# Optimization experiments

Hardware: AMD Instinct MI355X
Metric: run time of the kernel (lower is better)

The kernel has to match this reference:

```python
import jax, jax.numpy as jnp
import numpy as np

NUM_EMBEDDINGS = 512
EMBEDDING_DIM = 64
COMMITMENT_COST = 0.25


def setup_inputs() -> dict:
    key = jax.random.key(0)
    k1, k2 = jax.random.split(key)
    inputs = jax.random.normal(k1, (64, 32, 32, EMBEDDING_DIM), dtype=jnp.float32)
    # nn.Embedding weight init: uniform(-1/K, 1/K)
    codebook = jax.random.uniform(
        k2, (NUM_EMBEDDINGS, EMBEDDING_DIM), dtype=jnp.float32,
        minval=-1.0 / NUM_EMBEDDINGS, maxval=1.0 / NUM_EMBEDDINGS)
    return {"inputs": inputs, "codebook": codebook}


def reference(inputs, codebook):
    D = codebook.shape[1]
    K = codebook.shape[0]
    flat = inputs.reshape(-1, D)  # [N, D]
    # Squared euclidean distances (argmin-equivalent to torch.cdist output)
    d2 = (jnp.sum(flat * flat, axis=1, keepdims=True)
          - 2.0 * (flat @ codebook.T)
          + jnp.sum(codebook * codebook, axis=1))  # [N, K]
    idx = jnp.argmin(d2, axis=1)  # [N]
    # Gather codebook rows (== one-hot @ codebook in the original)
    quantized = codebook[idx].reshape(inputs.shape)
    e_latent_loss = jnp.mean((jax.lax.stop_gradient(quantized) - inputs) ** 2)
    q_latent_loss = jnp.mean((quantized - jax.lax.stop_gradient(inputs)) ** 2)
    loss = q_latent_loss + COMMITMENT_COST * e_latent_loss
    # Straight-through estimator
    quantized_st = inputs + jax.lax.stop_gradient(quantized - inputs)
    # Perplexity from code usage histogram (== mean of one-hot encodings)
    n = flat.shape[0]
    avg_probs = jnp.zeros((K,), dtype=jnp.float32).at[idx].add(1.0) / n
    perplexity = jnp.exp(-jnp.sum(avg_probs * jnp.log(avg_probs + 1e-10)))
    encoding_indices = idx[:, None]  # [N, 1] to match torch unsqueeze(1)
    return (loss, quantized_st, perplexity, encoding_indices)
```

## Files before the change

kernel.cpp:

```cpp
#include <hip/hip_runtime.h>
#include <math.h>

#define K_EMB 512
#define DIM 64
#define NVEC 65536
#define OUT_LOSS 0
#define OUT_Q 1
#define OUT_PERP (1 + NVEC * DIM)
#define OUT_IDX (1 + NVEC * DIM + 1)
#define EPS2 1e-4f
#define FIX_CAP 16
#define GRID_MAIN 2048
#define SSE_SLOTS 32

typedef __attribute__((ext_vector_type(8))) short short8;
typedef __attribute__((ext_vector_type(4))) float float4v;


__device__ __forceinline__ unsigned short bf16_rn(float f) {
    unsigned u = __float_as_uint(f);
    return (unsigned short)((u + 0x7FFFu + ((u >> 16) & 1u)) >> 16);
}

__device__ __forceinline__ float np_pairwise8_sq(const float* v) {
    float r[8];
#pragma unroll
    for (int j = 0; j < 8; ++j) r[j] = __fmul_rn(v[j], v[j]);
#pragma unroll
    for (int i = 8; i < 64; i += 8) {
#pragma unroll
        for (int j = 0; j < 8; ++j) r[j] = __fadd_rn(r[j], __fmul_rn(v[i + j], v[i + j]));
    }
    return __fadd_rn(__fadd_rn(__fadd_rn(r[0], r[1]), __fadd_rn(r[2], r[3])),
                     __fadd_rn(__fadd_rn(r[4], r[5]), __fadd_rn(r[6], r[7])));
}

__device__ __forceinline__ float np_pairwise8_sq_g(const float* g) {
    float x[64];
    const float4* v4 = (const float4*)g;
#pragma unroll
    for (int i = 0; i < 16; ++i) {
        float4 t = v4[i];
        x[4 * i + 0] = t.x; x[4 * i + 1] = t.y; x[4 * i + 2] = t.z; x[4 * i + 3] = t.w;
    }
    float r[8];
#pragma unroll
    for (int j = 0; j < 8; ++j) r[j] = __fmul_rn(x[j], x[j]);
#pragma unroll
    for (int i = 8; i < 64; i += 8) {
#pragma unroll
        for (int j = 0; j < 8; ++j) r[j] = __fadd_rn(r[j], __fmul_rn(x[i + j], x[i + j]));
    }
    return __fadd_rn(__fadd_rn(__fadd_rn(r[0], r[1]), __fadd_rn(r[2], r[3])),
                     __fadd_rn(__fadd_rn(r[4], r[5]), __fadd_rn(r[6], r[7])));
}

__global__ void vq_frag(const float* __restrict__ codebook, float* __restrict__ csq,
                        unsigned short* __restrict__ ahi, unsigned short* __restrict__ alo,
                        float4* __restrict__ csqf, unsigned* __restrict__ hist,
                        double* __restrict__ sse64, unsigned* __restrict__ cnt) {
    const int tid = threadIdx.x;
    if (blockIdx.x < 16) {
        const int id = blockIdx.x * 256 + tid;
        const int t = id >> 7, step = (id >> 6) & 1, lane = id & 63;
        const int m = t * 16 + (lane & 15);
        const int kb = step * 32 + (lane >> 4) * 8;
        const float4* src = (const float4*)(codebook + (m << 6) + kb);
        float4 f0 = src[0], f1 = src[1];
        const float fs[8] = {f0.x, f0.y, f0.z, f0.w, f1.x, f1.y, f1.z, f1.w};
        short8 h, l;
#pragma unroll
        for (int j = 0; j < 8; ++j) {
            unsigned short hv = bf16_rn(fs[j]);
            float lof = fs[j] - __uint_as_float(((unsigned)hv) << 16);
            h[j] = (short)hv;
            l[j] = (short)bf16_rn(lof);
        }
        const int fo = ((t * 2 + step) * 64 + lane) * 8;
        *(short8*)(ahi + fo) = h;
        *(short8*)(alo + fo) = l;
    } else {
        __shared__ float s_csq[512];
#pragma unroll
        for (int r = 0; r < 2; ++r) {
            const int k = tid + 256 * r;
            float v = np_pairwise8_sq_g(codebook + ((size_t)k << 6));
            s_csq[k] = v;
            csq[k] = v;
            hist[k] = 0u;
        }
        if (tid < SSE_SLOTS) sse64[tid] = 0.0;
        if (tid == SSE_SLOTS) *cnt = 0u;
        __syncthreads();
#pragma unroll
        for (int i = 0; i < 8; ++i) {
            const int id = i * 256 + tid;
            const int t = id >> 6, lane = id & 63;
            const int k0 = t * 16 + (lane >> 4) * 4;
            csqf[id] = make_float4(s_csq[k0], s_csq[k0 + 1], s_csq[k0 + 2], s_csq[k0 + 3]);
        }
    }
}

__launch_bounds__(256, 4)
__global__ void vq_main(const float* __restrict__ inputs, const float* __restrict__ codebook,
                        const float* __restrict__ csq, const unsigned short* __restrict__ ahi,
                        const unsigned short* __restrict__ alo, const float4* __restrict__ csqf,
                        unsigned* __restrict__ hist, double* __restrict__ sse64,
                        unsigned* __restrict__ cnt, float* __restrict__ out) {
    __shared__ __align__(16) float s_x[32 * 68];
    __shared__ float s_A[32];
    __shared__ unsigned long long s_t1[4][32];
    __shared__ unsigned long long s_t2[4][32];
    __shared__ unsigned long long s_e[32];
    __shared__ int s_fix[FIX_CAP];
    __shared__ int s_nfix;
    __shared__ float s_w[4];
    __shared__ int s_last;
    __shared__ float s_wsm[8];
    __shared__ double s_sse[SSE_SLOTS];

    const int tid = threadIdx.x;
    const int wave = tid >> 6, lane = tid & 63;
    const int vbase = blockIdx.x * 32;

    if (tid == 0) s_nfix = 0;

    {
        const float4* src = (const float4*)(inputs + ((size_t)vbase << 6));
#pragma unroll
        for (int i = 0; i < 2; ++i) {
            const int f = i * 256 + tid;
            float4 v = src[f];
            *(float4*)&s_x[(f >> 4) * 68 + (f & 15) * 4] = v;
        }
    }
    __syncthreads();

    if (tid < 32) s_A[tid] = np_pairwise8_sq(&s_x[tid * 68]);
    __syncthreads();

    short8 bhi[2][2], blo[2][2];
#pragma unroll
    for (int vt = 0; vt < 2; ++vt) {
        const int vrow = vt * 16 + (lane & 15);
#pragma unroll
        for (int step = 0; step < 2; ++step) {
            const int kb = step * 32 + (lane >> 4) * 8;
            float4 f0 = *(const float4*)&s_x[vrow * 68 + kb];
            float4 f1 = *(const float4*)&s_x[vrow * 68 + kb + 4];
            const float fs[8] = {f0.x, f0.y, f0.z, f0.w, f1.x, f1.y, f1.z, f1.w};
            short8 h, l;
#pragma unroll
            for (int j = 0; j < 8; ++j) {
                unsigned short hv = bf16_rn(fs[j]);
                float lof = fs[j] - __uint_as_float(((unsigned)hv) << 16);
                h[j] = (short)hv;
                l[j] = (short)bf16_rn(lof);
            }
            bhi[vt][step] = h;
            blo[vt][step] = l;
        }
    }

    unsigned long long e1[2] = {~0ULL, ~0ULL}, e2[2] = {~0ULL, ~0ULL};

#pragma unroll 2
    for (int tt = 0; tt < 8; ++tt) {
        const int t = wave * 8 + tt;
        const int fo0 = ((t * 2 + 0) * 64 + lane) * 8;
        const int fo1 = ((t * 2 + 1) * 64 + lane) * 8;
        short8 ah0 = *(const short8*)(ahi + fo0);
        short8 ah1 = *(const short8*)(ahi + fo1);
        short8 al0 = *(const short8*)(alo + fo0);
        short8 al1 = *(const short8*)(alo + fo1);
        float4 cs = csqf[t * 64 + lane];
        const float csr[4] = {cs.x, cs.y, cs.z, cs.w};
#pragma unroll
        for (int vt = 0; vt < 2; ++vt) {
            float4v acc = {0.f, 0.f, 0.f, 0.f};
            acc = __builtin_amdgcn_mfma_f32_16x16x32_bf16(ah0, bhi[vt][0], acc, 0, 0, 0);
            acc = __builtin_amdgcn_mfma_f32_16x16x32_bf16(ah1, bhi[vt][1], acc, 0, 0, 0);
            acc = __builtin_amdgcn_mfma_f32_16x16x32_bf16(ah0, blo[vt][0], acc, 0, 0, 0);
            acc = __builtin_amdgcn_mfma_f32_16x16x32_bf16(ah1, blo[vt][1], acc, 0, 0, 0);
            acc = __builtin_amdgcn_mfma_f32_16x16x32_bf16(al0, bhi[vt][0], acc, 0, 0, 0);
            acc = __builtin_amdgcn_mfma_f32_16x16x32_bf16(al1, bhi[vt][1], acc, 0, 0, 0);
            const float Avt = s_A[vt * 16 + (lane & 15)];
#pragma unroll
            for (int r = 0; r < 4; ++r) {
                float d2 = __fadd_rn(__fsub_rn(Avt, __fmul_rn(2.0f, acc[r])), csr[r]);
                const unsigned k = (unsigned)(t * 16 + (lane >> 4) * 4 + r);
                unsigned long long e = ((unsigned long long)__float_as_uint(d2) << 32) | k;
                if (e < e1[vt]) { e2[vt] = e1[vt]; e1[vt] = e; }
                else if (e < e2[vt]) e2[vt] = e;
            }
        }
    }

#pragma unroll
    for (int vt = 0; vt < 2; ++vt) {
#pragma unroll
        for (int off = 16; off <= 32; off <<= 1) {
            unsigned long long o1 = __shfl_xor(e1[vt], off);
            unsigned long long o2 = __shfl_xor(e2[vt], off);
            if (o1 < e1[vt]) { e2[vt] = (e1[vt] < o2) ? e1[vt] : o2; e1[vt] = o1; }
            else if (o1 < e2[vt]) e2[vt] = o1;
        }
        if (lane < 16) {
            s_t1[wave][vt * 16 + lane] = e1[vt];
            s_t2[wave][vt * 16 + lane] = e2[vt];
        }
    }
    __syncthreads();

    if (tid < 32) {
        unsigned long long E1 = ~0ULL, E2 = ~0ULL;
#pragma unroll
        for (int w = 0; w < 4; ++w) {
            unsigned long long a = s_t1[w][tid], b = s_t2[w][tid];
            if (a < E1) { E2 = (E1 < b) ? E1 : b; E1 = a; }
            else if (a < E2) E2 = a;
        }
        s_e[tid] = E1;
        float b1 = __uint_as_float((unsigned)(E1 >> 32));
        float b2 = __uint_as_float((unsigned)(E2 >> 32));
        if (__fsub_rn(b2, b1) <= EPS2) {
            int pos = atomicAdd(&s_nfix, 1);
            if (pos < FIX_CAP) s_fix[pos] = tid;
        }
    }
    __syncthreads();

    {
        int nf = s_nfix; if (nf > FIX_CAP) nf = FIX_CAP;
        for (int f = wave; f < nf; f += 4) {
            const int vloc = s_fix[f];
            const float* xr = &s_x[vloc * 68];
            const float A = s_A[vloc];
            unsigned long long best = ~0ULL;
#pragma unroll 1
            for (int r8 = 0; r8 < 8; ++r8) {
                const int k = lane * 8 + r8;
                const float* c = codebook + (k << 6);
                float p[8] = {0.f, 0.f, 0.f, 0.f, 0.f, 0.f, 0.f, 0.f};
#pragma unroll
                for (int ii = 0; ii < 64; ii += 8)
#pragma unroll
                    for (int j = 0; j < 8; ++j)
                        p[j] = __builtin_fmaf(xr[ii + j], c[ii + j], p[j]);
                float dot = __fadd_rn(__fadd_rn(__fadd_rn(p[0], p[1]), __fadd_rn(p[2], p[3])),
                                      __fadd_rn(__fadd_rn(p[4], p[5]), __fadd_rn(p[6], p[7])));
                float d2 = __fadd_rn(__fsub_rn(A, __fmul_rn(2.0f, dot)), csq[k]);
                unsigned long long e = ((unsigned long long)__float_as_uint(d2) << 32) | (unsigned)k;
                if (e < best) best = e;
            }
#pragma unroll
            for (int off = 32; off > 0; off >>= 1) {
                unsigned long long o = __shfl_down(best, off);
                if (o < best) best = o;
            }
            if (lane == 0) s_e[vloc] = best;
        }
    }
    __syncthreads();

    if (tid < 32) {
        const unsigned kf = (unsigned)s_e[tid];
        out[OUT_IDX + vbase + tid] = (float)kf;
        atomicAdd(&hist[kf], 1u);
    }
    {
        float4* dst = (float4*)(out + OUT_Q + ((size_t)vbase << 6));
        float es = 0.f;
#pragma unroll
        for (int i = 0; i < 2; ++i) {
            const int f = i * 256 + tid;
            const int row = f >> 4, col = (f & 15) * 4;
            const unsigned k = (unsigned)s_e[row];
            float4 qv = *(const float4*)(codebook + ((size_t)k << 6) + col);
            dst[f] = qv;
            float4 xv = *(const float4*)&s_x[row * 68 + col];
            float d0 = qv.x - xv.x; es = __builtin_fmaf(d0, d0, es);
            float d1 = qv.y - xv.y; es = __builtin_fmaf(d1, d1, es);
            float d2 = qv.z - xv.z; es = __builtin_fmaf(d2, d2, es);
            float d3 = qv.w - xv.w; es = __builtin_fmaf(d3, d3, es);
        }
#pragma unroll
        for (int off = 32; off > 0; off >>= 1) es += __shfl_down(es, off);
        if (lane == 0) s_w[wave] = es;
    }
    __syncthreads();
    if (tid == 0) {
        atomicAdd(&sse64[blockIdx.x & (SSE_SLOTS - 1)],
                  (double)(((s_w[0] + s_w[1]) + (s_w[2] + s_w[3]))));
        asm volatile("s_waitcnt vmcnt(0)" ::: "memory");
        unsigned ticket = atomicAdd(cnt, 1u);
        s_last = (ticket == GRID_MAIN - 1) ? 1 : 0;
    }
    __syncthreads();

    if (s_last) {
        float pr0 = (float)atomicAdd(&hist[tid], 0u) / 65536.0f;
        float v0 = __fmul_rn(pr0, logf(__fadd_rn(pr0, 1e-10f)));
        float pr1 = (float)atomicAdd(&hist[tid + 256], 0u) / 65536.0f;
        float v1 = __fmul_rn(pr1, logf(__fadd_rn(pr1, 1e-10f)));
#pragma unroll
        for (int off = 32; off > 0; off >>= 1) {
            v0 += __shfl_down(v0, off);
            v1 += __shfl_down(v1, off);
        }
        if (lane == 0) { s_wsm[wave] = v0; s_wsm[4 + wave] = v1; }
        if (tid < SSE_SLOTS) s_sse[tid] = atomicAdd(&sse64[tid], 0.0);
        __syncthreads();
        if (tid == 0) {
            float S = 0.f;
#pragma unroll
            for (int i = 0; i < 8; ++i) S += s_wsm[i];
            out[OUT_PERP] = expf(-S);
            double sv = 0.0;
            for (int i = 0; i < SSE_SLOTS; ++i) sv += s_sse[i];
            float m = (float)(sv / 4194304.0);
            out[OUT_LOSS] = __fadd_rn(m, __fmul_rn(0.25f, m));
        }
    }
}

extern "C" void kernel_launch(void* const* d_in, const int* in_sizes, int n_in,
                              void* d_out, int out_size, void* d_ws, size_t ws_size,
                              hipStream_t stream) {
    const float* inputs   = (const float*)d_in[0];
    const float* codebook = (const float*)d_in[1];
    float* out = (float*)d_out;
    float*          csq   = (float*)d_ws;
    double*         sse64 = (double*)((char*)d_ws + 2048);
    unsigned*       cnt   = (unsigned*)((char*)d_ws + 2304);
    unsigned*       hist  = (unsigned*)((char*)d_ws + 2560);
    unsigned short* ahi   = (unsigned short*)((char*)d_ws + 4608);
    unsigned short* alo   = (unsigned short*)((char*)d_ws + 70144);
    float4*         csqf  = (float4*)((char*)d_ws + 135680);

    vq_frag<<<17, 256, 0, stream>>>(codebook, csq, ahi, alo, csqf, hist, sse64, cnt);
    vq_main<<<GRID_MAIN, 256, 0, stream>>>(inputs, codebook, csq, ahi, alo, csqf, hist, sse64, cnt, out);
}
```

Before: 137.1 us.

## Use single-wave blocks covering all codes with software-pipelined codebook fragment loads

Each block now runs one wave that sweeps all 32 codebook tiles instead of splitting them across four waves. This removes the __syncthreads barriers and the cross-wave top-2 merge through shared memory. Fragment loads are double-buffered with a per-block rotation of the starting tile, the row norms come from in-register FMA plus shuffles, and the distance becomes a single fma. The trade-off is more serial MFMA work per wave and fewer waves per block. The changed norm and distance arithmetic may also shift near-tie results, though the fixup path still recomputes ties exactly.

```diff
diff --git a/kernel.cpp b/kernel.cpp
--- a/kernel.cpp
+++ b/kernel.cpp
@@ -102,45 +102,36 @@
     }
 }
 
-__launch_bounds__(256, 4)
+__launch_bounds__(64, 2)
 __global__ void vq_main(const float* __restrict__ inputs, const float* __restrict__ codebook,
                         const float* __restrict__ csq, const unsigned short* __restrict__ ahi,
                         const unsigned short* __restrict__ alo, const float4* __restrict__ csqf,
                         unsigned* __restrict__ hist, double* __restrict__ sse64,
                         unsigned* __restrict__ cnt, float* __restrict__ out) {
     __shared__ __align__(16) float s_x[32 * 68];
-    __shared__ float s_A[32];
-    __shared__ unsigned long long s_t1[4][32];
-    __shared__ unsigned long long s_t2[4][32];
     __shared__ unsigned long long s_e[32];
     __shared__ int s_fix[FIX_CAP];
     __shared__ int s_nfix;
-    __shared__ float s_w[4];
-    __shared__ int s_last;
     __shared__ float s_wsm[8];
     __shared__ double s_sse[SSE_SLOTS];
 
-    const int tid = threadIdx.x;
-    const int wave = tid >> 6, lane = tid & 63;
+    const int lane = threadIdx.x;
     const int vbase = blockIdx.x * 32;
 
-    if (tid == 0) s_nfix = 0;
+    if (lane == 0) s_nfix = 0;
 
     {
         const float4* src = (const float4*)(inputs + ((size_t)vbase << 6));
 #pragma unroll
-        for (int i = 0; i < 2; ++i) {
-            const int f = i * 256 + tid;
+        for (int i = 0; i < 8; ++i) {
+            const int f = i * 64 + lane;
             float4 v = src[f];
             *(float4*)&s_x[(f >> 4) * 68 + (f & 15) * 4] = v;
         }
     }
-    __syncthreads();
-
-    if (tid < 32) s_A[tid] = np_pairwise8_sq(&s_x[tid * 68]);
-    __syncthreads();
 
     short8 bhi[2][2], blo[2][2];
+    float A2[2] = {0.f, 0.f};
 #pragma unroll
     for (int vt = 0; vt < 2; ++vt) {
         const int vrow = vt * 16 + (lane & 15);
@@ -153,6 +144,7 @@
             short8 h, l;
 #pragma unroll
             for (int j = 0; j < 8; ++j) {
+                A2[vt] = __builtin_fmaf(fs[j], fs[j], A2[vt]);
                 unsigned short hv = bf16_rn(fs[j]);
                 float lof = fs[j] - __uint_as_float(((unsigned)hv) << 16);
                 h[j] = (short)hv;
@@ -161,39 +153,61 @@
             bhi[vt][step] = h;
             blo[vt][step] = l;
         }
+        A2[vt] += __shfl_xor(A2[vt], 16);
+        A2[vt] += __shfl_xor(A2[vt], 32);
     }
 
     unsigned long long e1[2] = {~0ULL, ~0ULL}, e2[2] = {~0ULL, ~0ULL};
-
-#pragma unroll 2
-    for (int tt = 0; tt < 8; ++tt) {
-        const int t = wave * 8 + tt;
-        const int fo0 = ((t * 2 + 0) * 64 + lane) * 8;
-        const int fo1 = ((t * 2 + 1) * 64 + lane) * 8;
-        short8 ah0 = *(const short8*)(ahi + fo0);
-        short8 ah1 = *(const short8*)(ahi + fo1);
-        short8 al0 = *(const short8*)(alo + fo0);
-        short8 al1 = *(const short8*)(alo + fo1);
-        float4 cs = csqf[t * 64 + lane];
-        const float csr[4] = {cs.x, cs.y, cs.z, cs.w};
-#pragma unroll
-        for (int vt = 0; vt < 2; ++vt) {
-            float4v acc = {0.f, 0.f, 0.f, 0.f};
-            acc = __builtin_amdgcn_mfma_f32_16x16x32_bf16(ah0, bhi[vt][0], acc, 0, 0, 0);
-            acc = __builtin_amdgcn_mfma_f32_16x16x32_bf16(ah1, bhi[vt][1], acc, 0, 0, 0);
-            acc = __builtin_amdgcn_mfma_f32_16x16x32_bf16(ah0, blo[vt][0], acc, 0, 0, 0);
-            acc = __builtin_amdgcn_mfma_f32_16x16x32_bf16(ah1, blo[vt][1], acc, 0, 0, 0);
-            acc = __builtin_amdgcn_mfma_f32_16x16x32_bf16(al0, bhi[vt][0], acc, 0, 0, 0);
-            acc = __builtin_amdgcn_mfma_f32_16x16x32_bf16(al1, bhi[vt][1], acc, 0, 0, 0);
-            const float Avt = s_A[vt * 16 + (lane & 15)];
-#pragma unroll
-            for (int r = 0; r < 4; ++r) {
-                float d2 = __fadd_rn(__fsub_rn(Avt, __fmul_rn(2.0f, acc[r])), csr[r]);
-                const unsigned k = (unsigned)(t * 16 + (lane >> 4) * 4 + r);
-                unsigned long long e = ((unsigned long long)__float_as_uint(d2) << 32) | k;
-                if (e < e1[vt]) { e2[vt] = e1[vt]; e1[vt] = e; }
-                else if (e < e2[vt]) e2[vt] = e;
-            }
+    const int rot = (int)(blockIdx.x & 31);
+
+#define LOADT(tv, d0, d1, d2_, d3, d4) {                                    \
+        const int t_ = (tv);                                                \
+        const int fo0_ = ((t_ * 2 + 0) * 64 + lane) * 8;                    \
+        const int fo1_ = ((t_ * 2 + 1) * 64 + lane) * 8;                    \
+        d0 = *(const short8*)(ahi + fo0_);                                  \
+        d1 = *(const short8*)(ahi + fo1_);                                  \
+        d2_ = *(const short8*)(alo + fo0_);                                 \
+        d3 = *(const short8*)(alo + fo1_);                                  \
+        d4 = csqf[t_ * 64 + lane]; }
+
+#define COMPT(tv, ah0, ah1, al0, al1, cs) {                                 \
+        const int t_ = (tv);                                                \
+        const float csr_[4] = {cs.x, cs.y, cs.z, cs.w};                     \
+        _Pragma("unroll")                                                   \
+        for (int vt = 0; vt < 2; ++vt) {                                    \
+            float4v acc = {0.f, 0.f, 0.f, 0.f};                             \
+            acc = __builtin_amdgcn_mfma_f32_16x16x32_bf16(ah0, bhi[vt][0], acc, 0, 0, 0); \
+            acc = __builtin_amdgcn_mfma_f32_16x16x32_bf16(ah1, bhi[vt][1], acc, 0, 0, 0); \
+            acc = __builtin_amdgcn_mfma_f32_16x16x32_bf16(ah0, blo[vt][0], acc, 0, 0, 0); \
+            acc = __builtin_amdgcn_mfma_f32_16x16x32_bf16(ah1, blo[vt][1], acc, 0, 0, 0); \
+            acc = __builtin_amdgcn_mfma_f32_16x16x32_bf16(al0, bhi[vt][0], acc, 0, 0, 0); \
+            acc = __builtin_amdgcn_mfma_f32_16x16x32_bf16(al1, bhi[vt][1], acc, 0, 0, 0); \
+            const float Avt = A2[vt];                                       \
+            float pc_[4];                                                   \
+            _Pragma("unroll")                                               \
+            for (int r = 0; r < 4; ++r) pc_[r] = __fadd_rn(Avt, csr_[r]);   \
+            _Pragma("unroll")                                               \
+            for (int r = 0; r < 4; ++r) {                                   \
+                  \
+                float d2 = __builtin_fmaf(-2.0f, acc[r], pc_[r]);           \
+                const unsigned k = (unsigned)(t_ * 16 + (lane >> 4) * 4 + r); \
+                unsigned long long e = ((unsigned long long)__float_as_uint(d2) << 32) | k; \
+                if (e < e1[vt]) { e2[vt] = e1[vt]; e1[vt] = e; }            \
+                else if (e < e2[vt]) e2[vt] = e;                            \
+            }                                                               \
+        } }
+
+    {
+        short8 aA0, aA1, aA2, aA3; float4 cA;
+        short8 aB0, aB1, aB2, aB3; float4 cB;
+        LOADT(rot, aA0, aA1, aA2, aA3, cA);
+#pragma unroll 1
+        for (int tp = 0; tp < 16; ++tp) {
+            const int i0 = 2 * tp, i1 = 2 * tp + 1;
+            LOADT((i1 + rot) & 31, aB0, aB1, aB2, aB3, cB);
+            COMPT((i0 + rot) & 31, aA0, aA1, aA2, aA3, cA);
+            if (tp < 15) LOADT((i1 + 1 + rot) & 31, aA0, aA1, aA2, aA3, cA);
+            COMPT((i1 + rot) & 31, aB0, aB1, aB2, aB3, cB);
         }
     }
 
@@ -207,36 +221,22 @@
             else if (o1 < e2[vt]) e2[vt] = o1;
         }
         if (lane < 16) {
-            s_t1[wave][vt * 16 + lane] = e1[vt];
-            s_t2[wave][vt * 16 + lane] = e2[vt];
-        }
-    }
-    __syncthreads();
-
-    if (tid < 32) {
-        unsigned long long E1 = ~0ULL, E2 = ~0ULL;
-#pragma unroll
-        for (int w = 0; w < 4; ++w) {
-            unsigned long long a = s_t1[w][tid], b = s_t2[w][tid];
-            if (a < E1) { E2 = (E1 < b) ? E1 : b; E1 = a; }
-            else if (a < E2) E2 = a;
-        }
-        s_e[tid] = E1;
-        float b1 = __uint_as_float((unsigned)(E1 >> 32));
-        float b2 = __uint_as_float((unsigned)(E2 >> 32));
-        if (__fsub_rn(b2, b1) <= EPS2) {
-            int pos = atomicAdd(&s_nfix, 1);
-            if (pos < FIX_CAP) s_fix[pos] = tid;
-        }
-    }
-    __syncthreads();
+            s_e[vt * 16 + lane] = e1[vt];
+            float b1 = __uint_as_float((unsigned)(e1[vt] >> 32));
+            float b2 = __uint_as_float((unsigned)(e2[vt] >> 32));
+            if (__fsub_rn(b2, b1) <= EPS2) {
+                int pos = atomicAdd(&s_nfix, 1);
+                if (pos < FIX_CAP) s_fix[pos] = vt * 16 + lane;
+            }
+        }
+    }
 
     {
         int nf = s_nfix; if (nf > FIX_CAP) nf = FIX_CAP;
-        for (int f = wave; f < nf; f += 4) {
+        for (int f = 0; f < nf; ++f) {
             const int vloc = s_fix[f];
             const float* xr = &s_x[vloc * 68];
-            const float A = s_A[vloc];
+            const float A = np_pairwise8_sq(xr);
             unsigned long long best = ~0ULL;
 #pragma unroll 1
             for (int r8 = 0; r8 < 8; ++r8) {
@@ -262,19 +262,18 @@
             if (lane == 0) s_e[vloc] = best;
         }
     }
-    __syncthreads();
-
-    if (tid < 32) {
-        const unsigned kf = (unsigned)s_e[tid];
-        out[OUT_IDX + vbase + tid] = (float)kf;
+
+    if (lane < 32) {
+        const unsigned kf = (unsigned)s_e[lane];
+        out[OUT_IDX + vbase + lane] = (float)kf;
         atomicAdd(&hist[kf], 1u);
     }
+    float es = 0.f;
     {
         float4* dst = (float4*)(out + OUT_Q + ((size_t)vbase << 6));
-        float es = 0.f;
-#pragma unroll
-        for (int i = 0; i < 2; ++i) {
-            const int f = i * 256 + tid;
+#pragma unroll
+        for (int i = 0; i < 8; ++i) {
+            const int f = i * 64 + lane;
             const int row = f >> 4, col = (f & 15) * 4;
             const unsigned k = (unsigned)s_e[row];
             float4 qv = *(const float4*)(codebook + ((size_t)k << 6) + col);
@@ -287,32 +286,26 @@
         }
 #pragma unroll
         for (int off = 32; off > 0; off >>= 1) es += __shfl_down(es, off);
-        if (lane == 0) s_w[wave] = es;
-    }
-    __syncthreads();
-    if (tid == 0) {
-        atomicAdd(&sse64[blockIdx.x & (SSE_SLOTS - 1)],
-                  (double)(((s_w[0] + s_w[1]) + (s_w[2] + s_w[3]))));
-        asm volatile("s_waitcnt vmcnt(0)" ::: "memory");
-        unsigned ticket = atomicAdd(cnt, 1u);
-        s_last = (ticket == GRID_MAIN - 1) ? 1 : 0;
-    }
-    __syncthreads();
-
-    if (s_last) {
-        float pr0 = (float)atomicAdd(&hist[tid], 0u) / 65536.0f;
-        float v0 = __fmul_rn(pr0, logf(__fadd_rn(pr0, 1e-10f)));
-        float pr1 = (float)atomicAdd(&hist[tid + 256], 0u) / 65536.0f;
-        float v1 = __fmul_rn(pr1, logf(__fadd_rn(pr1, 1e-10f)));
-#pragma unroll
-        for (int off = 32; off > 0; off >>= 1) {
-            v0 += __shfl_down(v0, off);
-            v1 += __shfl_down(v1, off);
-        }
-        if (lane == 0) { s_wsm[wave] = v0; s_wsm[4 + wave] = v1; }
-        if (tid < SSE_SLOTS) s_sse[tid] = atomicAdd(&sse64[tid], 0.0);
-        __syncthreads();
-        if (tid == 0) {
+    }
+
+    asm volatile("s_waitcnt vmcnt(0)" ::: "memory");
+    if (lane == 0) atomicAdd(&sse64[blockIdx.x & (SSE_SLOTS - 1)], (double)es);
+    asm volatile("s_waitcnt vmcnt(0)" ::: "memory");
+    unsigned tk = 0u;
+    if (lane == 0) tk = atomicAdd(cnt, 1u);
+    tk = __shfl(tk, 0);
+
+    if (tk == GRID_MAIN - 1) {
+#pragma unroll 1
+        for (int c = 0; c < 8; ++c) {
+            float pr = (float)atomicAdd(&hist[c * 64 + lane], 0u) / 65536.0f;
+            float v = __fmul_rn(pr, logf(__fadd_rn(pr, 1e-10f)));
+#pragma unroll
+            for (int off = 32; off > 0; off >>= 1) v += __shfl_down(v, off);
+            if (lane == 0) s_wsm[c] = v;
+        }
+        if (lane < SSE_SLOTS) s_sse[lane] = atomicAdd(&sse64[lane], 0.0);
+        if (lane == 0) {
             float S = 0.f;
 #pragma unroll
             for (int i = 0; i < 8; ++i) S += s_wsm[i];
@@ -323,6 +316,8 @@
             out[OUT_LOSS] = __fadd_rn(m, __fmul_rn(0.25f, m));
         }
     }
+#undef LOADT
+#undef COMPT
 }
 
 extern "C" void kernel_launch(void* const* d_in, const int* in_sizes, int n_in,
@@ -340,5 +335,5 @@
     float4*         csqf  = (float4*)((char*)d_ws + 135680);
 
     vq_frag<<<17, 256, 0, stream>>>(codebook, csq, ahi, alo, csqf, hist, sse64, cnt);
-    vq_main<<<GRID_MAIN, 256, 0, stream>>>(inputs, codebook, csq, ahi, alo, csqf, hist, sse64, cnt, out);
-}
+    vq_main<<<GRID_MAIN, 64, 0, stream>>>(inputs, codebook, csq, ahi, alo, csqf, hist, sse64, cnt, out);
+}
```

After: 147.7 us. +7.8%, slower.

## Compute norms in registers, skip fix-up barriers on common path, wave-level finalize

Applied to the files above, without the earlier changes.

Each block now computes input squared norms in registers during the bf16 split, which removes the s_A shared-memory pass and a barrier. It precomputes A+csq so each distance is one fma, and rotates the codebook tile order per block to spread L2 reads. Near-tie detection uses a wave ballot, so blocks with no ties skip the exact-recompute path and its barriers. The final reduction uses per-wave atomics and a shared counter instead of block barriers. The risks are changed rounding in A and d2, which can flip near-tie argmins, and a subtle per-wave completion protocol.

```diff
diff --git a/kernel.cpp b/kernel.cpp
--- a/kernel.cpp
+++ b/kernel.cpp
@@ -9,7 +9,6 @@
 #define OUT_PERP (1 + NVEC * DIM)
 #define OUT_IDX (1 + NVEC * DIM + 1)
 #define EPS2 1e-4f
-#define FIX_CAP 16
 #define GRID_MAIN 2048
 #define SSE_SLOTS 32
 
@@ -109,14 +108,10 @@
                         unsigned* __restrict__ hist, double* __restrict__ sse64,
                         unsigned* __restrict__ cnt, float* __restrict__ out) {
     __shared__ __align__(16) float s_x[32 * 68];
-    __shared__ float s_A[32];
     __shared__ unsigned long long s_t1[4][32];
     __shared__ unsigned long long s_t2[4][32];
     __shared__ unsigned long long s_e[32];
-    __shared__ int s_fix[FIX_CAP];
-    __shared__ int s_nfix;
-    __shared__ float s_w[4];
-    __shared__ int s_last;
+    __shared__ unsigned s_done;
     __shared__ float s_wsm[8];
     __shared__ double s_sse[SSE_SLOTS];
 
@@ -124,7 +119,7 @@
     const int wave = tid >> 6, lane = tid & 63;
     const int vbase = blockIdx.x * 32;
 
-    if (tid == 0) s_nfix = 0;
+    if (tid == 0) s_done = 0u;
 
     {
         const float4* src = (const float4*)(inputs + ((size_t)vbase << 6));
@@ -137,10 +132,8 @@
     }
     __syncthreads();
 
-    if (tid < 32) s_A[tid] = np_pairwise8_sq(&s_x[tid * 68]);
-    __syncthreads();
-
     short8 bhi[2][2], blo[2][2];
+    float A2[2] = {0.f, 0.f};
 #pragma unroll
     for (int vt = 0; vt < 2; ++vt) {
         const int vrow = vt * 16 + (lane & 15);
@@ -153,6 +146,7 @@
             short8 h, l;
 #pragma unroll
             for (int j = 0; j < 8; ++j) {
+                A2[vt] = __builtin_fmaf(fs[j], fs[j], A2[vt]);
                 unsigned short hv = bf16_rn(fs[j]);
                 float lof = fs[j] - __uint_as_float(((unsigned)hv) << 16);
                 h[j] = (short)hv;
@@ -161,13 +155,16 @@
             bhi[vt][step] = h;
             blo[vt][step] = l;
         }
+        A2[vt] += __shfl_xor(A2[vt], 16);
+        A2[vt] += __shfl_xor(A2[vt], 32);
     }
 
     unsigned long long e1[2] = {~0ULL, ~0ULL}, e2[2] = {~0ULL, ~0ULL};
+    const int rot = (int)(blockIdx.x & 7);
 
 #pragma unroll 2
     for (int tt = 0; tt < 8; ++tt) {
-        const int t = wave * 8 + tt;
+        const int t = wave * 8 + ((tt + rot) & 7);
         const int fo0 = ((t * 2 + 0) * 64 + lane) * 8;
         const int fo1 = ((t * 2 + 1) * 64 + lane) * 8;
         short8 ah0 = *(const short8*)(ahi + fo0);
@@ -185,10 +182,13 @@
             acc = __builtin_amdgcn_mfma_f32_16x16x32_bf16(ah1, blo[vt][1], acc, 0, 0, 0);
             acc = __builtin_amdgcn_mfma_f32_16x16x32_bf16(al0, bhi[vt][0], acc, 0, 0, 0);
             acc = __builtin_amdgcn_mfma_f32_16x16x32_bf16(al1, bhi[vt][1], acc, 0, 0, 0);
-            const float Avt = s_A[vt * 16 + (lane & 15)];
+            const float Avt = A2[vt];
+            float pc[4];
+#pragma unroll
+            for (int r = 0; r < 4; ++r) pc[r] = __fadd_rn(Avt, csr[r]);
 #pragma unroll
             for (int r = 0; r < 4; ++r) {
-                float d2 = __fadd_rn(__fsub_rn(Avt, __fmul_rn(2.0f, acc[r])), csr[r]);
+                float d2 = __builtin_fmaf(-2.0f, acc[r], pc[r]);
                 const unsigned k = (unsigned)(t * 16 + (lane >> 4) * 4 + r);
                 unsigned long long e = ((unsigned long long)__float_as_uint(d2) << 32) | k;
                 if (e < e1[vt]) { e2[vt] = e1[vt]; e1[vt] = e; }
@@ -213,30 +213,53 @@
     }
     __syncthreads();
 
-    if (tid < 32) {
-        unsigned long long E1 = ~0ULL, E2 = ~0ULL;
+    unsigned long long E1 = ~0ULL, E2 = ~0ULL;
+    {
+        const int v = lane & 31;
 #pragma unroll
         for (int w = 0; w < 4; ++w) {
-            unsigned long long a = s_t1[w][tid], b = s_t2[w][tid];
+            unsigned long long a = s_t1[w][v], b = s_t2[w][v];
             if (a < E1) { E2 = (E1 < b) ? E1 : b; E1 = a; }
             else if (a < E2) E2 = a;
         }
-        s_e[tid] = E1;
-        float b1 = __uint_as_float((unsigned)(E1 >> 32));
-        float b2 = __uint_as_float((unsigned)(E2 >> 32));
-        if (__fsub_rn(b2, b1) <= EPS2) {
-            int pos = atomicAdd(&s_nfix, 1);
-            if (pos < FIX_CAP) s_fix[pos] = tid;
-        }
-    }
-    __syncthreads();
-
-    {
-        int nf = s_nfix; if (nf > FIX_CAP) nf = FIX_CAP;
+    }
+    const float b1 = __uint_as_float((unsigned)(E1 >> 32));
+    const float b2 = __uint_as_float((unsigned)(E2 >> 32));
+    const unsigned long long mask =
+        __ballot(lane < 32 && __fsub_rn(b2, b1) <= EPS2);
+
+    float es = 0.f;
+    float4* dst = (float4*)(out + OUT_Q + ((size_t)vbase << 6));
+
+    if (mask == 0ULL) {
+        if (tid < 32) {
+            const unsigned kf = (unsigned)E1;
+            out[OUT_IDX + vbase + tid] = (float)kf;
+            atomicAdd(&hist[kf], 1u);
+        }
+#pragma unroll
+        for (int i = 0; i < 2; ++i) {
+            const int f = i * 256 + tid;
+            const int row = f >> 4, col = (f & 15) * 4;
+            const unsigned k = (unsigned)__shfl(E1, row);
+            float4 qv = *(const float4*)(codebook + ((size_t)k << 6) + col);
+            dst[f] = qv;
+            float4 xv = *(const float4*)&s_x[row * 68 + col];
+            float d0 = qv.x - xv.x; es = __builtin_fmaf(d0, d0, es);
+            float d1 = qv.y - xv.y; es = __builtin_fmaf(d1, d1, es);
+            float d2 = qv.z - xv.z; es = __builtin_fmaf(d2, d2, es);
+            float d3 = qv.w - xv.w; es = __builtin_fmaf(d3, d3, es);
+        }
+    } else {
+        if (lane < 32) s_e[lane] = E1;
+        __syncthreads();
+        const int nf = __popcll(mask);
         for (int f = wave; f < nf; f += 4) {
-            const int vloc = s_fix[f];
+            unsigned long long mm = mask;
+            for (int i = 0; i < f; ++i) mm &= mm - 1;
+            const int vloc = __ffsll((long long)mm) - 1;
             const float* xr = &s_x[vloc * 68];
-            const float A = s_A[vloc];
+            const float A = np_pairwise8_sq(xr);
             unsigned long long best = ~0ULL;
 #pragma unroll 1
             for (int r8 = 0; r8 < 8; ++r8) {
@@ -261,17 +284,12 @@
             }
             if (lane == 0) s_e[vloc] = best;
         }
-    }
-    __syncthreads();
-
-    if (tid < 32) {
-        const unsigned kf = (unsigned)s_e[tid];
-        out[OUT_IDX + vbase + tid] = (float)kf;
-        atomicAdd(&hist[kf], 1u);
-    }
-    {
-        float4* dst = (float4*)(out + OUT_Q + ((size_t)vbase << 6));
-        float es = 0.f;
+        __syncthreads();
+        if (tid < 32) {
+            const unsigned kf = (unsigned)s_e[tid];
+            out[OUT_IDX + vbase + tid] = (float)kf;
+            atomicAdd(&hist[kf], 1u);
+        }
 #pragma unroll
         for (int i = 0; i < 2; ++i) {
             const int f = i * 256 + tid;
@@ -285,42 +303,41 @@
             float d2 = qv.z - xv.z; es = __builtin_fmaf(d2, d2, es);
             float d3 = qv.w - xv.w; es = __builtin_fmaf(d3, d3, es);
         }
-#pragma unroll
-        for (int off = 32; off > 0; off >>= 1) es += __shfl_down(es, off);
-        if (lane == 0) s_w[wave] = es;
-    }
-    __syncthreads();
-    if (tid == 0) {
-        atomicAdd(&sse64[blockIdx.x & (SSE_SLOTS - 1)],
-                  (double)(((s_w[0] + s_w[1]) + (s_w[2] + s_w[3]))));
-        asm volatile("s_waitcnt vmcnt(0)" ::: "memory");
-        unsigned ticket = atomicAdd(cnt, 1u);
-        s_last = (ticket == GRID_MAIN - 1) ? 1 : 0;
-    }
-    __syncthreads();
-
-    if (s_last) {
-        float pr0 = (float)atomicAdd(&hist[tid], 0u) / 65536.0f;
-        float v0 = __fmul_rn(pr0, logf(__fadd_rn(pr0, 1e-10f)));
-        float pr1 = (float)atomicAdd(&hist[tid + 256], 0u) / 65536.0f;
-        float v1 = __fmul_rn(pr1, logf(__fadd_rn(pr1, 1e-10f)));
-#pragma unroll
-        for (int off = 32; off > 0; off >>= 1) {
-            v0 += __shfl_down(v0, off);
-            v1 += __shfl_down(v1, off);
-        }
-        if (lane == 0) { s_wsm[wave] = v0; s_wsm[4 + wave] = v1; }
-        if (tid < SSE_SLOTS) s_sse[tid] = atomicAdd(&sse64[tid], 0.0);
-        __syncthreads();
-        if (tid == 0) {
-            float S = 0.f;
-#pragma unroll
-            for (int i = 0; i < 8; ++i) S += s_wsm[i];
-            out[OUT_PERP] = expf(-S);
-            double sv = 0.0;
-            for (int i = 0; i < SSE_SLOTS; ++i) sv += s_sse[i];
-            float m = (float)(sv / 4194304.0);
-            out[OUT_LOSS] = __fadd_rn(m, __fmul_rn(0.25f, m));
+    }
+
+#pragma unroll
+    for (int off = 32; off > 0; off >>= 1) es += __shfl_down(es, off);
+
+    asm volatile("s_waitcnt vmcnt(0)" ::: "memory");
+    if (lane == 0) atomicAdd(&sse64[blockIdx.x & (SSE_SLOTS - 1)], (double)es);
+    asm volatile("s_waitcnt vmcnt(0)" ::: "memory");
+    unsigned dn = 0u;
+    if (lane == 0) dn = atomicAdd(&s_done, 1u);
+    dn = __shfl(dn, 0);
+    if (dn == 3u) {
+        unsigned tk = 0u;
+        if (lane == 0) tk = atomicAdd(cnt, 1u);
+        tk = __shfl(tk, 0);
+        if (tk == GRID_MAIN - 1u) {
+#pragma unroll 1
+            for (int c = 0; c < 8; ++c) {
+                float pr = (float)atomicAdd(&hist[c * 64 + lane], 0u) / 65536.0f;
+                float v = __fmul_rn(pr, logf(__fadd_rn(pr, 1e-10f)));
+#pragma unroll
+                for (int off = 32; off > 0; off >>= 1) v += __shfl_down(v, off);
+                if (lane == 0) s_wsm[c] = v;
+            }
+            if (lane < SSE_SLOTS) s_sse[lane] = atomicAdd(&sse64[lane], 0.0);
+            if (lane == 0) {
+                float S = 0.f;
+#pragma unroll
+                for (int i = 0; i < 8; ++i) S += s_wsm[i];
+                out[OUT_PERP] = expf(-S);
+                double sv = 0.0;
+                for (int i = 0; i < SSE_SLOTS; ++i) sv += s_sse[i];
+                float m = (float)(sv / 4194304.0);
+                out[OUT_LOSS] = __fadd_rn(m, __fmul_rn(0.25f, m));
+            }
         }
     }
 }
```

After: 147.0 us. +7.2%, slower.

## Shrink vq_main blocks to 16 vectors with two waves each

Applied to the files above, without the earlier changes.

Each block now handles 16 input vectors with 128 threads (two waves) instead of 32 vectors with four waves, and the grid doubles to 4096 blocks. Each wave sweeps 256 codes for a single 16-vector tile, so the per-wave codebook fragments from global memory are reused across one tile instead of two. The aim is more blocks and less per-thread register state for better latency hiding. The cost is twice the codebook fragment traffic per input vector and more per-block overhead (atomics, syncs, ticket counting).

```diff
diff --git a/kernel.cpp b/kernel.cpp
--- a/kernel.cpp
+++ b/kernel.cpp
@@ -10,7 +10,7 @@
 #define OUT_IDX (1 + NVEC * DIM + 1)
 #define EPS2 1e-4f
 #define FIX_CAP 16
-#define GRID_MAIN 2048
+#define GRID_MAIN 4096
 #define SSE_SLOTS 32
 
 typedef __attribute__((ext_vector_type(8))) short short8;
@@ -102,27 +102,27 @@
     }
 }
 
-__launch_bounds__(256, 4)
+__launch_bounds__(128, 8)
 __global__ void vq_main(const float* __restrict__ inputs, const float* __restrict__ codebook,
                         const float* __restrict__ csq, const unsigned short* __restrict__ ahi,
                         const unsigned short* __restrict__ alo, const float4* __restrict__ csqf,
                         unsigned* __restrict__ hist, double* __restrict__ sse64,
                         unsigned* __restrict__ cnt, float* __restrict__ out) {
-    __shared__ __align__(16) float s_x[32 * 68];
-    __shared__ float s_A[32];
-    __shared__ unsigned long long s_t1[4][32];
-    __shared__ unsigned long long s_t2[4][32];
-    __shared__ unsigned long long s_e[32];
+    __shared__ __align__(16) float s_x[16 * 68];
+    __shared__ float s_A[16];
+    __shared__ unsigned long long s_t1[2][16];
+    __shared__ unsigned long long s_t2[2][16];
+    __shared__ unsigned long long s_e[16];
     __shared__ int s_fix[FIX_CAP];
     __shared__ int s_nfix;
-    __shared__ float s_w[4];
+    __shared__ float s_w[2];
     __shared__ int s_last;
     __shared__ float s_wsm[8];
     __shared__ double s_sse[SSE_SLOTS];
 
     const int tid = threadIdx.x;
     const int wave = tid >> 6, lane = tid & 63;
-    const int vbase = blockIdx.x * 32;
+    const int vbase = blockIdx.x * 16;
 
     if (tid == 0) s_nfix = 0;
 
@@ -130,20 +130,19 @@
         const float4* src = (const float4*)(inputs + ((size_t)vbase << 6));
 #pragma unroll
         for (int i = 0; i < 2; ++i) {
-            const int f = i * 256 + tid;
+            const int f = i * 128 + tid;
             float4 v = src[f];
             *(float4*)&s_x[(f >> 4) * 68 + (f & 15) * 4] = v;
         }
     }
     __syncthreads();
 
-    if (tid < 32) s_A[tid] = np_pairwise8_sq(&s_x[tid * 68]);
-    __syncthreads();
-
-    short8 bhi[2][2], blo[2][2];
-#pragma unroll
-    for (int vt = 0; vt < 2; ++vt) {
-        const int vrow = vt * 16 + (lane & 15);
+    if (tid < 16) s_A[tid] = np_pairwise8_sq(&s_x[tid * 68]);
+    __syncthreads();
+
+    short8 bhi[2], blo[2];
+    {
+        const int vrow = lane & 15;
 #pragma unroll
         for (int step = 0; step < 2; ++step) {
             const int kb = step * 32 + (lane >> 4) * 8;
@@ -158,16 +157,16 @@
                 h[j] = (short)hv;
                 l[j] = (short)bf16_rn(lof);
             }
-            bhi[vt][step] = h;
-            blo[vt][step] = l;
-        }
-    }
-
-    unsigned long long e1[2] = {~0ULL, ~0ULL}, e2[2] = {~0ULL, ~0ULL};
+            bhi[step] = h;
+            blo[step] = l;
+        }
+    }
+
+    unsigned long long e1 = ~0ULL, e2 = ~0ULL;
 
 #pragma unroll 2
-    for (int tt = 0; tt < 8; ++tt) {
-        const int t = wave * 8 + tt;
+    for (int tt = 0; tt < 16; ++tt) {
+        const int t = wave * 16 + tt;
         const int fo0 = ((t * 2 + 0) * 64 + lane) * 8;
         const int fo1 = ((t * 2 + 1) * 64 + lane) * 8;
         short8 ah0 = *(const short8*)(ahi + fo0);
@@ -176,47 +175,43 @@
         short8 al1 = *(const short8*)(alo + fo1);
         float4 cs = csqf[t * 64 + lane];
         const float csr[4] = {cs.x, cs.y, cs.z, cs.w};
-#pragma unroll
-        for (int vt = 0; vt < 2; ++vt) {
-            float4v acc = {0.f, 0.f, 0.f, 0.f};
-            acc = __builtin_amdgcn_mfma_f32_16x16x32_bf16(ah0, bhi[vt][0], acc, 0, 0, 0);
-            acc = __builtin_amdgcn_mfma_f32_16x16x32_bf16(ah1, bhi[vt][1], acc, 0, 0, 0);
-            acc = __builtin_amdgcn_mfma_f32_16x16x32_bf16(ah0, blo[vt][0], acc, 0, 0, 0);
-            acc = __builtin_amdgcn_mfma_f32_16x16x32_bf16(ah1, blo[vt][1], acc, 0, 0, 0);
-            acc = __builtin_amdgcn_mfma_f32_16x16x32_bf16(al0, bhi[vt][0], acc, 0, 0, 0);
-            acc = __builtin_amdgcn_mfma_f32_16x16x32_bf16(al1, bhi[vt][1], acc, 0, 0, 0);
-            const float Avt = s_A[vt * 16 + (lane & 15)];
-#pragma unroll
-            for (int r = 0; r < 4; ++r) {
-                float d2 = __fadd_rn(__fsub_rn(Avt, __fmul_rn(2.0f, acc[r])), csr[r]);
-                const unsigned k = (unsigned)(t * 16 + (lane >> 4) * 4 + r);
-                unsigned long long e = ((unsigned long long)__float_as_uint(d2) << 32) | k;
-                if (e < e1[vt]) { e2[vt] = e1[vt]; e1[vt] = e; }
-                else if (e < e2[vt]) e2[vt] = e;
-            }
-        }
-    }
-
-#pragma unroll
-    for (int vt = 0; vt < 2; ++vt) {
+        float4v acc = {0.f, 0.f, 0.f, 0.f};
+        acc = __builtin_amdgcn_mfma_f32_16x16x32_bf16(ah0, bhi[0], acc, 0, 0, 0);
+        acc = __builtin_amdgcn_mfma_f32_16x16x32_bf16(ah1, bhi[1], acc, 0, 0, 0);
+        acc = __builtin_amdgcn_mfma_f32_16x16x32_bf16(ah0, blo[0], acc, 0, 0, 0);
+        acc = __builtin_amdgcn_mfma_f32_16x16x32_bf16(ah1, blo[1], acc, 0, 0, 0);
+        acc = __builtin_amdgcn_mfma_f32_16x16x32_bf16(al0, bhi[0], acc, 0, 0, 0);
+        acc = __builtin_amdgcn_mfma_f32_16x16x32_bf16(al1, bhi[1], acc, 0, 0, 0);
+        const float Avt = s_A[lane & 15];
+#pragma unroll
+        for (int r = 0; r < 4; ++r) {
+            float d2 = __fadd_rn(__fsub_rn(Avt, __fmul_rn(2.0f, acc[r])), csr[r]);
+            const unsigned k = (unsigned)(t * 16 + (lane >> 4) * 4 + r);
+            unsigned long long e = ((unsigned long long)__float_as_uint(d2) << 32) | k;
+            if (e < e1) { e2 = e1; e1 = e; }
+            else if (e < e2) e2 = e;
+        }
+    }
+
+    {
 #pragma unroll
         for (int off = 16; off <= 32; off <<= 1) {
-            unsigned long long o1 = __shfl_xor(e1[vt], off);
-            unsigned long long o2 = __shfl_xor(e2[vt], off);
-            if (o1 < e1[vt]) { e2[vt] = (e1[vt] < o2) ? e1[vt] : o2; e1[vt] = o1; }
-            else if (o1 < e2[vt]) e2[vt] = o1;
+            unsigned long long o1 = __shfl_xor(e1, off);
+            unsigned long long o2 = __shfl_xor(e2, off);
+            if (o1 < e1) { e2 = (e1 < o2) ? e1 : o2; e1 = o1; }
+            else if (o1 < e2) e2 = o1;
         }
         if (lane < 16) {
-            s_t1[wave][vt * 16 + lane] = e1[vt];
-            s_t2[wave][vt * 16 + lane] = e2[vt];
-        }
-    }
-    __syncthreads();
-
-    if (tid < 32) {
+            s_t1[wave][lane] = e1;
+            s_t2[wave][lane] = e2;
+        }
+    }
+    __syncthreads();
+
+    if (tid < 16) {
         unsigned long long E1 = ~0ULL, E2 = ~0ULL;
 #pragma unroll
-        for (int w = 0; w < 4; ++w) {
+        for (int w = 0; w < 2; ++w) {
             unsigned long long a = s_t1[w][tid], b = s_t2[w][tid];
             if (a < E1) { E2 = (E1 < b) ? E1 : b; E1 = a; }
             else if (a < E2) E2 = a;
@@ -233,7 +228,7 @@
 
     {
         int nf = s_nfix; if (nf > FIX_CAP) nf = FIX_CAP;
-        for (int f = wave; f < nf; f += 4) {
+        for (int f = wave; f < nf; f += 2) {
             const int vloc = s_fix[f];
             const float* xr = &s_x[vloc * 68];
             const float A = s_A[vloc];
@@ -264,7 +259,7 @@
     }
     __syncthreads();
 
-    if (tid < 32) {
+    if (tid < 16) {
         const unsigned kf = (unsigned)s_e[tid];
         out[OUT_IDX + vbase + tid] = (float)kf;
         atomicAdd(&hist[kf], 1u);
@@ -274,7 +269,7 @@
         float es = 0.f;
 #pragma unroll
         for (int i = 0; i < 2; ++i) {
-            const int f = i * 256 + tid;
+            const int f = i * 128 + tid;
             const int row = f >> 4, col = (f & 15) * 4;
             const unsigned k = (unsigned)s_e[row];
             float4 qv = *(const float4*)(codebook + ((size_t)k << 6) + col);
@@ -292,7 +287,7 @@
     __syncthreads();
     if (tid == 0) {
         atomicAdd(&sse64[blockIdx.x & (SSE_SLOTS - 1)],
-                  (double)(((s_w[0] + s_w[1]) + (s_w[2] + s_w[3]))));
+                  (double)(s_w[0] + s_w[1]));
         asm volatile("s_waitcnt vmcnt(0)" ::: "memory");
         unsigned ticket = atomicAdd(cnt, 1u);
         s_last = (ticket == GRID_MAIN - 1) ? 1 : 0;
@@ -300,16 +295,15 @@
     __syncthreads();
 
     if (s_last) {
-        float pr0 = (float)atomicAdd(&hist[tid], 0u) / 65536.0f;
-        float v0 = __fmul_rn(pr0, logf(__fadd_rn(pr0, 1e-10f)));
-        float pr1 = (float)atomicAdd(&hist[tid + 256], 0u) / 65536.0f;
-        float v1 = __fmul_rn(pr1, logf(__fadd_rn(pr1, 1e-10f)));
-#pragma unroll
-        for (int off = 32; off > 0; off >>= 1) {
-            v0 += __shfl_down(v0, off);
-            v1 += __shfl_down(v1, off);
-        }
-        if (lane == 0) { s_wsm[wave] = v0; s_wsm[4 + wave] = v1; }
+#pragma unroll 1
+        for (int r = 0; r < 4; ++r) {
+            const int c = r * 2 + wave;
+            float pr = (float)atomicAdd(&hist[c * 64 + lane], 0u) / 65536.0f;
+            float v = __fmul_rn(pr, logf(__fadd_rn(pr, 1e-10f)));
+#pragma unroll
+            for (int off = 32; off > 0; off >>= 1) v += __shfl_down(v, off);
+            if (lane == 0) s_wsm[c] = v;
+        }
         if (tid < SSE_SLOTS) s_sse[tid] = atomicAdd(&sse64[tid], 0.0);
         __syncthreads();
         if (tid == 0) {
@@ -340,5 +334,5 @@
     float4*         csqf  = (float4*)((char*)d_ws + 135680);
 
     vq_frag<<<17, 256, 0, stream>>>(codebook, csq, ahi, alo, csqf, hist, sse64, cnt);
-    vq_main<<<GRID_MAIN, 256, 0, stream>>>(inputs, codebook, csq, ahi, alo, csqf, hist, sse64, cnt, out);
-}
+    vq_main<<<GRID_MAIN, 128, 0, stream>>>(inputs, codebook, csq, ahi, alo, csqf, hist, sse64, cnt, out);
+}
```

Measured after the change: 216.9 us. +58.2%, slower.
